# Optimization experiments

Hardware: AMD Instinct MI355X
Metric: run time of the kernel (lower is better)

The kernel has to match this reference:

```python
import jax, jax.numpy as jnp
import numpy as np
from itertools import permutations

N_NODES, B, C, H, W = 3, 4, 256, 40, 40
NO_PASS = 2


def _conv3x3(x, w, b):
    # x: [NB, Cin, H, W], w: [Cout, Cin, 3, 3]
    y = jax.lax.conv_general_dilated(
        x, w, window_strides=(1, 1), padding='SAME',
        dimension_numbers=('NCHW', 'OIHW', 'NCHW'))
    return y + b[None, :, None, None]


def setup_inputs() -> dict:
    key = jax.random.key(0)
    ks = jax.random.split(key, 7)
    s = 0.02
    return {
        'nodes': jax.random.normal(ks[0], (N_NODES, B, C, H, W), jnp.float32),
        'theta_w': jax.random.normal(ks[1], (C, C), jnp.float32) * s,
        'theta_b': jax.random.normal(ks[2], (C,), jnp.float32) * s,
        'gru_gates_w': jax.random.normal(ks[3], (2 * C, 2 * C, 3, 3), jnp.float32) * s,
        'gru_gates_b': jax.random.normal(ks[4], (2 * C,), jnp.float32) * s,
        'gru_can_w': jax.random.normal(ks[5], (C, 2 * C, 3, 3), jnp.float32) * s,
        'gru_can_b': jax.random.normal(ks[6], (C,), jnp.float32) * s,
    }


def reference(nodes, theta_w, theta_b, gru_gates_w, gru_gates_b, gru_can_w, gru_can_b):
    N, Bn, Cn, Hn, Wn = nodes.shape
    P = Hn * Wn
    edges = np.array(list(permutations(range(N), 2)))  # [E, 2]
    recv = jnp.asarray(edges[:, 0])  # edge[0] receives message
    send = jnp.asarray(edges[:, 1])  # edge[1] sends

    for _ in range(NO_PASS):
        nf = nodes.reshape(N, Bn, Cn, P)
        # theta is a 1x1 conv == channel matmul
        th = jnp.einsum('oc,nbcp->nbop', theta_w, nf) + theta_b[None, None, :, None]
        thi = th[recv]          # [E, B, C, P]
        ei = nf[recv]           # [E, B, C, P]
        ej = nf[send]           # [E, B, C, P]
        # scores[e,b,p,q] = theta(e1)[:,p] . e2[:,q]
        scores = jnp.einsum('ebcp,ebcq->ebpq', thi, ej)
        atn = jax.nn.softmax(scores, axis=-1)
        # message = atn @ (e2 + e1)^T, back to channel-first
        msg = jnp.einsum('ebpq,ebcq->ebcp', atn, ej + ei)  # [E, B, C, P]
        agg = jax.ops.segment_sum(msg, recv, num_segments=N)  # sum of incoming msgs

        # ConvGRU update, nodes folded into batch dim
        x = agg.reshape(N * Bn, Cn, Hn, Wn)
        h = nodes.reshape(N * Bn, Cn, Hn, Wn)
        gates = _conv3x3(jnp.concatenate([x, h], axis=1), gru_gates_w, gru_gates_b)
        r, z = jnp.split(jax.nn.sigmoid(gates), 2, axis=1)
        cand = jnp.tanh(_conv3x3(jnp.concatenate([x, r * h], axis=1), gru_can_w, gru_can_b))
        h_new = (1.0 - z) * h + z * cand
        nodes = h_new.reshape(N, Bn, Cn, Hn, Wn)
    return nodes
```

## Files before the change

kernel.cpp:

```cpp
#include <hip/hip_runtime.h>
#include <hip/hip_bf16.h>
#include <math.h>

#define NN 3
#define BB 4
#define CC 256
#define C2 512
#define HH 40
#define WW 40
#define PP 1600
#define NBB 12
#define NODESZ (NBB*CC*PP)
#define TO 16
#define PAD 1764

typedef short short8 __attribute__((ext_vector_type(8)));
typedef float f32x4 __attribute__((ext_vector_type(4)));
typedef unsigned short ushort_t;
typedef unsigned int uint_t;

__device__ __forceinline__ ushort_t f2bf(float x) {
  union { float f; uint_t u; } v; v.f = x;
  uint_t r = v.u + 0x7fff + ((v.u >> 16) & 1);
  return (ushort_t)(r >> 16);
}

__device__ __forceinline__ void async_ld16(const ushort_t* g, ushort_t* l) {
  __builtin_amdgcn_global_load_lds(
      (const __attribute__((address_space(1))) uint_t*)g,
      (__attribute__((address_space(3))) uint_t*)l, 16, 0, 0);
}

__global__ void k_copy(const float* __restrict__ in, float* __restrict__ out) {
  int i = blockIdx.x * 256 + threadIdx.x;
  out[i] = in[i];
}

__global__ void k_theta(const float* __restrict__ nodes, const float* __restrict__ tw,
                        const float* __restrict__ tb, ushort_t* __restrict__ th_t) {
  __shared__ float w[TO * CC];
  int t = threadIdx.x;
  int nb = blockIdx.y / (CC / TO);
  int o0 = (blockIdx.y % (CC / TO)) * TO;
  for (int i = t; i < TO * CC; i += 320) w[i] = tw[(o0 + (i >> 8)) * CC + (i & 255)];
  __syncthreads();
  int p = blockIdx.x * 320 + t;
  const float* src = nodes + nb * CC * PP + p;
  float acc[TO];
#pragma unroll
  for (int o = 0; o < TO; ++o) acc[o] = tb[o0 + o];
  for (int c = 0; c < CC; c += 4) {
    float v0 = src[c * PP], v1 = src[(c + 1) * PP], v2 = src[(c + 2) * PP], v3 = src[(c + 3) * PP];
#pragma unroll
    for (int o = 0; o < TO; ++o) {
      const float4 ww = *(const float4*)(w + o * CC + c);
      acc[o] += ww.x * v0 + ww.y * v1 + ww.z * v2 + ww.w * v3;
    }
  }
  size_t base = ((size_t)nb * PP + p) * CC + o0;
#pragma unroll
  for (int o = 0; o < TO; o += 2) {
    uint_t lo = f2bf(acc[o]), hi = f2bf(acc[o + 1]);
    *(uint_t*)&th_t[base + o] = lo | (hi << 16);
  }
}

__global__ void k_to_bf_t(const float* __restrict__ src, ushort_t* __restrict__ dst) {
  __shared__ float tile[32][33];
  int nb = blockIdx.z;
  int c0 = blockIdx.y * 32;
  int pp0 = blockIdx.x * 32;
  int tx = threadIdx.x & 31, ty = threadIdx.x >> 5;
#pragma unroll
  for (int i = 0; i < 4; ++i)
    tile[ty + 8 * i][tx] = src[((size_t)nb * CC + c0 + ty + 8 * i) * PP + pp0 + tx];
  __syncthreads();
#pragma unroll
  for (int i = 0; i < 4; ++i) {
    int q = pp0 + ty + 8 * i;
    int c = c0 + tx;
    int cs = c ^ ((q & 7) << 3);
    dst[((size_t)nb * PP + q) * CC + cs] = f2bf(tile[tx][ty + 8 * i]);
  }
}

__global__ void k_prep_vf(const float* __restrict__ nodes, ushort_t* __restrict__ vf) {
  int T = blockIdx.x;
  int eb = blockIdx.y;
  int e = eb >> 2, b = eb & 3;
  int n = e >> 1, jidx = e & 1;
  int js = jidx + (jidx >= n ? 1 : 0);
  const float* s0 = nodes + (size_t)(n * BB + b) * CC * PP;
  const float* s1 = nodes + (size_t)(js * BB + b) * CC * PP;
  ushort_t* dst = vf + ((size_t)eb * 50 + T) * 8192;
  int t = threadIdx.x;
#pragma unroll
  for (int k = 0; k < 4; ++k) {
    int cid = t + 256 * k;
    int nt = cid >> 6, l = cid & 63;
    int quad = l >> 4, l16 = l & 15;
    int c = 16 * nt + l16;
    int p = 32 * T + quad * 8;
    const float4* a0 = (const float4*)(s0 + (size_t)c * PP + p);
    const float4* a1 = (const float4*)(s1 + (size_t)c * PP + p);
    float4 x0 = a0[0], x1 = a0[1];
    float4 y0 = a1[0], y1 = a1[1];
    short8 o;
    o[0] = (short)f2bf(x0.x + y0.x); o[1] = (short)f2bf(x0.y + y0.y);
    o[2] = (short)f2bf(x0.z + y0.z); o[3] = (short)f2bf(x0.w + y0.w);
    o[4] = (short)f2bf(x1.x + y1.x); o[5] = (short)f2bf(x1.y + y1.y);
    o[6] = (short)f2bf(x1.z + y1.z); o[7] = (short)f2bf(x1.w + y1.w);
    *(short8*)(dst + (size_t)cid * 8) = o;
  }
}

__global__ __launch_bounds__(256, 2) void k_attn_mfma(
    const ushort_t* __restrict__ nodes_bf_t,
    const ushort_t* __restrict__ th_t,
    const ushort_t* __restrict__ vf,
    float* __restrict__ agg_t)
{
  __shared__ ushort_t Ej[32 * 256];
  __shared__ ushort_t Sp[64 * 40];
  __shared__ float Al[64];
  __shared__ float Linv[64];

  const int t = threadIdx.x;
  const int w = t >> 6;
  const int l = t & 63;
  const int quad = l >> 4;
  const int l16 = l & 15;
  const int p0 = blockIdx.x * 64;
  const int nb = blockIdx.y;
  const int jidx = blockIdx.z;
  const int n = nb >> 2, b = nb & 3;
  const int e = n * 2 + jidx;
  const int js = jidx + (jidx >= n ? 1 : 0);
  const int eb = e * BB + b;

  const ushort_t* ejb = nodes_bf_t + ((size_t)(js * BB + b) * PP) * CC;
  const ushort_t* vbase = vf + (size_t)eb * 50 * 8192;

  short8 Ath[8];
  {
    const ushort_t* arow = th_t + ((size_t)nb * PP + p0 + 16 * w + l16) * CC + quad * 8;
#pragma unroll
    for (int ks = 0; ks < 8; ++ks) Ath[ks] = *(const short8*)(arow + ks * 32);
  }

  float M = -3.0e38f, Lr = 0.f;
  f32x4 O[4][4];
#pragma unroll
  for (int mt = 0; mt < 4; ++mt)
#pragma unroll
    for (int nt = 0; nt < 4; ++nt)
#pragma unroll
      for (int r = 0; r < 4; ++r) O[mt][nt][r] = 0.f;

#pragma unroll
  for (int i = 0; i < 4; ++i)
    async_ld16(ejb + (4 * w + i) * 512 + l * 8, &Ej[(4 * w + i) * 512]);

  for (int T = 0; T < 50; ++T) {
    __syncthreads();
    short8 Bv[4];
    {
      const ushort_t* vt = vbase + (size_t)T * 8192;
#pragma unroll
      for (int nt = 0; nt < 4; ++nt)
        Bv[nt] = *(const short8*)(vt + (4 * w + nt) * 512 + l * 8);
    }
    f32x4 S0, S1;
#pragma unroll
    for (int r = 0; r < 4; ++r) { S0[r] = 0.f; S1[r] = 0.f; }
#pragma unroll
    for (int ks = 0; ks < 8; ++ks) {
      int ch0 = (((ks * 4 + quad) ^ (l16 & 7)) << 3);
      short8 A0 = *(const short8*)(Ej + l16 * CC + ch0);
      short8 A1 = *(const short8*)(Ej + (16 + l16) * CC + ch0);
      S0 = __builtin_amdgcn_mfma_f32_16x16x32_bf16(A0, Ath[ks], S0, 0, 0, 0);
      S1 = __builtin_amdgcn_mfma_f32_16x16x32_bf16(A1, Ath[ks], S1, 0, 0, 0);
    }
    float m = fmaxf(fmaxf(fmaxf(S0[0], S0[1]), fmaxf(S0[2], S0[3])),
                    fmaxf(fmaxf(S1[0], S1[1]), fmaxf(S1[2], S1[3])));
    m = fmaxf(m, __shfl_xor(m, 16));
    m = fmaxf(m, __shfl_xor(m, 32));
    float Mn = fmaxf(M, m);
    float al = __expf(M - Mn);
    float e0 = __expf(S0[0] - Mn), e1 = __expf(S0[1] - Mn);
    float e2 = __expf(S0[2] - Mn), e3 = __expf(S0[3] - Mn);
    float e4 = __expf(S1[0] - Mn), e5 = __expf(S1[1] - Mn);
    float e6 = __expf(S1[2] - Mn), e7 = __expf(S1[3] - Mn);
    float s = ((e0 + e1) + (e2 + e3)) + ((e4 + e5) + (e6 + e7));
    s += __shfl_xor(s, 16);
    s += __shfl_xor(s, 32);
    Lr = Lr * al + s;
    M = Mn;
    {
      uint2 u;
      u.x = (uint_t)f2bf(e0) | ((uint_t)f2bf(e1) << 16);
      u.y = (uint_t)f2bf(e2) | ((uint_t)f2bf(e3) << 16);
      *(uint2*)&Sp[(16 * w + l16) * 40 + quad * 4] = u;
      uint2 v;
      v.x = (uint_t)f2bf(e4) | ((uint_t)f2bf(e5) << 16);
      v.y = (uint_t)f2bf(e6) | ((uint_t)f2bf(e7) << 16);
      *(uint2*)&Sp[(16 * w + l16) * 40 + 16 + quad * 4] = v;
      if (quad == 0) Al[16 * w + l16] = al;
    }
    __syncthreads();
    if (T < 49) {
#pragma unroll
      for (int i = 0; i < 4; ++i)
        async_ld16(ejb + (size_t)(T + 1) * 8192 + (4 * w + i) * 512 + l * 8,
                   &Ej[(4 * w + i) * 512]);
    }
#pragma unroll
    for (int mt = 0; mt < 4; ++mt) {
      f32x4 a4 = *(const f32x4*)&Al[16 * mt + quad * 4];
#pragma unroll
      for (int nt = 0; nt < 4; ++nt)
#pragma unroll
        for (int r = 0; r < 4; ++r) O[mt][nt][r] *= a4[r];
    }
#pragma unroll
    for (int mt = 0; mt < 4; ++mt) {
      short8 Ap = *(const short8*)&Sp[(16 * mt + l16) * 40 + quad * 8];
#pragma unroll
      for (int nt = 0; nt < 4; ++nt)
        O[mt][nt] = __builtin_amdgcn_mfma_f32_16x16x32_bf16(Ap, Bv[nt], O[mt][nt], 0, 0, 0);
    }
  }
  __syncthreads();
  if (quad == 0) Linv[16 * w + l16] = 1.f / Lr;
  __syncthreads();
  float* ao = agg_t + (((size_t)jidx * NBB + nb) * PP + p0) * CC;
#pragma unroll
  for (int mt = 0; mt < 4; ++mt) {
    f32x4 li = *(const f32x4*)&Linv[16 * mt + quad * 4];
#pragma unroll
    for (int r = 0; r < 4; ++r) {
      float* dst = ao + (size_t)(16 * mt + quad * 4 + r) * CC + 64 * w + l16;
#pragma unroll
      for (int nt = 0; nt < 4; ++nt) dst[16 * nt] = O[mt][nt][r] * li[r];
    }
  }
}


__global__ void k_wrep(const float* __restrict__ w, ushort_t* __restrict__ wr) {
  int i = blockIdx.x * 256 + threadIdx.x;
  int ci = i & 511;
  int rest = i >> 9;
  int tp = rest % 9, co = rest / 9;
  wr[i] = f2bf(w[((size_t)co * 512 + ci) * 9 + tp]);
}

__global__ void k_pad_zero(ushort_t* __restrict__ xpad) {
  int i = blockIdx.x * 256 + threadIdx.x;
  xpad[i] = 0;
}

__global__ void k_pad_agg(const float* __restrict__ agg_t, ushort_t* __restrict__ xpad) {
  int i = blockIdx.x * 256 + threadIdx.x;
  int c = i & 255;
  int rest = i >> 8;
  int px = rest % PP, nb = rest / PP;
  int y = px / 40, x = px - y * 40;
  size_t src = ((size_t)nb * PP + px) * CC + c;
  float v = agg_t[src] + agg_t[(size_t)NBB * PP * CC + src];
  xpad[((size_t)nb * PAD + (y + 1) * 42 + (x + 1)) * C2 + c] = f2bf(v);
}

template <int MODE>
__global__ void k_pad_tr(const float* __restrict__ srcA, const float* __restrict__ srcB,
                         ushort_t* __restrict__ xpad) {
  __shared__ float tile[32][33];
  int nb = blockIdx.z;
  int c0 = blockIdx.y * 32;
  int pp0 = blockIdx.x * 32;
  int tx = threadIdx.x & 31, ty = threadIdx.x >> 5;
#pragma unroll
  for (int i = 0; i < 4; ++i) {
    int c = c0 + ty + 8 * i;
    float v = srcA[((size_t)nb * CC + c) * PP + pp0 + tx];
    if (MODE == 1) v *= srcB[((size_t)nb * C2 + c) * PP + pp0 + tx];
    tile[ty + 8 * i][tx] = v;
  }
  __syncthreads();
#pragma unroll
  for (int i = 0; i < 4; ++i) {
    int px = pp0 + ty + 8 * i;
    int y = px / 40, x = px - y * 40;
    xpad[((size_t)nb * PAD + (y + 1) * 42 + (x + 1)) * C2 + CC + c0 + tx] =
        f2bf(tile[tx][ty + 8 * i]);
  }
}

template <int ACT>
__global__ __launch_bounds__(256) void k_conv_mfma(
    const ushort_t* __restrict__ xpad,
    const ushort_t* __restrict__ wr,
    const float* __restrict__ bias,
    const float* __restrict__ zsrc,
    float* __restrict__ out)
{
  __shared__ ushort_t Asm[128 * 32];
  __shared__ ushort_t Bsm[128 * 32];
  const int t = threadIdx.x;
  const int w = t >> 6, l = t & 63, quad = l >> 4, l16 = l & 15;
  const int nb = blockIdx.z;
  const int m0 = blockIdx.y * 128;
  const int px0 = blockIdx.x * 128;
  const int wm = (w >> 1) * 64, wn = (w & 1) * 64;

  const int lr = l >> 2;
  const int swf = (lr ^ (lr >> 2)) & 3;
  const int lk = ((l & 3) ^ swf) * 8;
  const ushort_t* wsrc = wr + (size_t)(m0 + 32 * w + lr) * 4608 + lk;
  int pxa = px0 + 32 * w + lr;      if (pxa > 1599) pxa = 1599;
  int pxb = pxa + 16;               if (pxb > 1599) pxb = 1599;
  {
    int d = px0 + 32 * w + 16 + lr; if (d <= 1599) pxb = d;
  }
  const int ya = pxa / 40, xa = pxa - ya * 40;
  const int yb = pxb / 40, xb = pxb - yb * 40;
  const ushort_t* bsrc_a = xpad + ((size_t)nb * PAD + ya * 42 + xa) * C2 + lk;
  const ushort_t* bsrc_b = xpad + ((size_t)nb * PAD + yb * 42 + xb) * C2 + lk;
  ushort_t* Ad0 = Asm + w * 1024;
  ushort_t* Ad1 = Asm + w * 1024 + 512;
  ushort_t* Bd0 = Bsm + w * 1024;
  ushort_t* Bd1 = Bsm + w * 1024 + 512;

  const int swr = (l16 ^ (l16 >> 2)) & 3;
  const int fk = ((quad ^ swr) * 8);

  f32x4 acc[4][4];
#pragma unroll
  for (int mt = 0; mt < 4; ++mt)
#pragma unroll
    for (int nt = 0; nt < 4; ++nt)
#pragma unroll
      for (int r = 0; r < 4; ++r) acc[mt][nt][r] = 0.f;

  for (int tap = 0; tap < 9; ++tap) {
    const int ky = tap / 3, kx = tap - ky * 3;
    const int boff = (ky * 42 + kx) * C2;
    const ushort_t* wtap = wsrc + tap * 512;
#pragma unroll 1
    for (int c0 = 0; c0 < 512; c0 += 32) {
      __syncthreads();
      async_ld16(wtap + c0, Ad0);
      async_ld16(wtap + 16 * 4608 + c0, Ad1);
      async_ld16(bsrc_a + boff + c0, Bd0);
      async_ld16(bsrc_b + boff + c0, Bd1);
      __syncthreads();
      short8 Af[4], Bf[4];
#pragma unroll
      for (int mt = 0; mt < 4; ++mt)
        Af[mt] = *(const short8*)(Asm + (wm + mt * 16 + l16) * 32 + fk);
#pragma unroll
      for (int nt = 0; nt < 4; ++nt)
        Bf[nt] = *(const short8*)(Bsm + (wn + nt * 16 + l16) * 32 + fk);
#pragma unroll
      for (int mt = 0; mt < 4; ++mt)
#pragma unroll
        for (int nt = 0; nt < 4; ++nt)
          acc[mt][nt] = __builtin_amdgcn_mfma_f32_16x16x32_bf16(Af[mt], Bf[nt], acc[mt][nt], 0, 0, 0);
    }
  }

#pragma unroll
  for (int mt = 0; mt < 4; ++mt) {
#pragma unroll
    for (int r = 0; r < 4; ++r) {
      int co = m0 + wm + mt * 16 + quad * 4 + r;
      float bv = bias[co];
#pragma unroll
      for (int nt = 0; nt < 4; ++nt) {
        int px = px0 + wn + nt * 16 + l16;
        if (px >= PP) continue;
        float v = acc[mt][nt][r] + bv;
        if (ACT == 0) {
          out[((size_t)nb * C2 + co) * PP + px] = 1.f / (1.f + __expf(-v));
        } else {
          v = tanhf(v);
          float z = zsrc[((size_t)nb * C2 + CC + co) * PP + px];
          float* hp = out + ((size_t)nb * CC + co) * PP + px;
          float h = *hp;
          *hp = (1.f - z) * h + z * v;
        }
      }
    }
  }
}

extern "C" void kernel_launch(void* const* d_in, const int* in_sizes, int n_in,
                              void* d_out, int out_size, void* d_ws, size_t ws_size,
                              hipStream_t stream) {
  const float* nodes_in = (const float*)d_in[0];
  const float* tw = (const float*)d_in[1];
  const float* tb = (const float*)d_in[2];
  const float* gw = (const float*)d_in[3];
  const float* gb = (const float*)d_in[4];
  const float* cw = (const float*)d_in[5];
  const float* cb = (const float*)d_in[6];

  float* nodes = (float*)d_out;
  char* ws = (char*)d_ws;
  ushort_t* nodes_bf_t = (ushort_t*)ws;
  ushort_t* th_t  = (ushort_t*)(ws + 9830400);
  ushort_t* vf    = (ushort_t*)(ws + 19660800);
  float*    agg_t = (float*)(ws + 39321600);
  ushort_t* xh_pad = (ushort_t*)(ws + 9830400);
  float*    gates = (float*)(ws + 39321600);
  ushort_t* w_g_r = (ushort_t*)(ws + 78643200);
  ushort_t* w_c_r = (ushort_t*)(ws + 83361792);

  k_copy<<<NODESZ / 256, 256, 0, stream>>>(nodes_in, nodes);
  k_wrep<<<(C2 * 9 * C2) / 256, 256, 0, stream>>>(gw, w_g_r);
  k_wrep<<<(CC * 9 * C2) / 256, 256, 0, stream>>>(cw, w_c_r);
  for (int pass = 0; pass < 2; ++pass) {
    k_theta<<<dim3(5, NBB * (CC / TO)), 320, 0, stream>>>(nodes, tw, tb, th_t);
    k_to_bf_t<<<dim3(50, 8, NBB), 256, 0, stream>>>(nodes, nodes_bf_t);
    k_prep_vf<<<dim3(50, 24), 256, 0, stream>>>(nodes, vf);
    k_attn_mfma<<<dim3(25, NBB, 2), 256, 0, stream>>>(nodes_bf_t, th_t, vf, agg_t);
    k_pad_zero<<<(NBB * PAD * C2) / 256, 256, 0, stream>>>(xh_pad);
    k_pad_agg<<<(NBB * PP * CC) / 256, 256, 0, stream>>>(agg_t, xh_pad);
    k_pad_tr<0><<<dim3(50, 8, NBB), 256, 0, stream>>>(nodes, nullptr, xh_pad);
    k_conv_mfma<0><<<dim3(13, 4, NBB), 256, 0, stream>>>(xh_pad, w_g_r, gb, nullptr, gates);
    k_pad_tr<1><<<dim3(50, 8, NBB), 256, 0, stream>>>(nodes, gates, xh_pad);
    k_conv_mfma<1><<<dim3(13, 2, NBB), 256, 0, stream>>>(xh_pad, w_c_r, cb, gates, nodes);
  }
}
```

Measured before the change: 1.107 ms.

## Double-buffer LDS tiles in MFMA conv to overlap loads with compute

Splits the A and B shared-memory tiles into two buffers and flattens the tap and channel loops into a single 144-step loop. Each step issues the async global-to-LDS loads for the next K-slice while the MFMAs run on the current slice. This leaves one barrier per step instead of two and is meant to hide global load latency. The cost is twice the LDS footprint, which may lower occupancy, and correctness relies on the barrier also waiting for the outstanding async loads.

Result: no change. 1.111 ms (+0.4%).

```diff
diff --git a/kernel.cpp b/kernel.cpp
--- a/kernel.cpp
+++ b/kernel.cpp
@@ -304,8 +304,8 @@
     const float* __restrict__ zsrc,
     float* __restrict__ out)
 {
-  __shared__ ushort_t Asm[128 * 32];
-  __shared__ ushort_t Bsm[128 * 32];
+  __shared__ ushort_t Asm[2][128 * 32];
+  __shared__ ushort_t Bsm[2][128 * 32];
   const int t = threadIdx.x;
   const int w = t >> 6, l = t & 63, quad = l >> 4, l16 = l & 15;
   const int nb = blockIdx.z;
@@ -326,10 +326,6 @@
   const int yb = pxb / 40, xb = pxb - yb * 40;
   const ushort_t* bsrc_a = xpad + ((size_t)nb * PAD + ya * 42 + xa) * C2 + lk;
   const ushort_t* bsrc_b = xpad + ((size_t)nb * PAD + yb * 42 + xb) * C2 + lk;
-  ushort_t* Ad0 = Asm + w * 1024;
-  ushort_t* Ad1 = Asm + w * 1024 + 512;
-  ushort_t* Bd0 = Bsm + w * 1024;
-  ushort_t* Bd1 = Bsm + w * 1024 + 512;
 
   const int swr = (l16 ^ (l16 >> 2)) & 3;
   const int fk = ((quad ^ swr) * 8);
@@ -342,31 +338,37 @@
 #pragma unroll
       for (int r = 0; r < 4; ++r) acc[mt][nt][r] = 0.f;
 
-  for (int tap = 0; tap < 9; ++tap) {
-    const int ky = tap / 3, kx = tap - ky * 3;
-    const int boff = (ky * 42 + kx) * C2;
-    const ushort_t* wtap = wsrc + tap * 512;
+  auto stage = [&](int buf, int it) {
+    int tap = it >> 4;
+    int cc = (it & 15) << 5;
+    int ky = tap / 3, kx = tap - ky * 3;
+    int boff = (ky * 42 + kx) * C2 + cc;
+    const ushort_t* wtap = wsrc + tap * 512 + cc;
+    async_ld16(wtap, &Asm[buf][w * 1024]);
+    async_ld16(wtap + 16 * 4608, &Asm[buf][w * 1024 + 512]);
+    async_ld16(bsrc_a + boff, &Bsm[buf][w * 1024]);
+    async_ld16(bsrc_b + boff, &Bsm[buf][w * 1024 + 512]);
+  };
+
+  stage(0, 0);
+  int cur = 0;
 #pragma unroll 1
-    for (int c0 = 0; c0 < 512; c0 += 32) {
-      __syncthreads();
-      async_ld16(wtap + c0, Ad0);
-      async_ld16(wtap + 16 * 4608 + c0, Ad1);
-      async_ld16(bsrc_a + boff + c0, Bd0);
-      async_ld16(bsrc_b + boff + c0, Bd1);
-      __syncthreads();
-      short8 Af[4], Bf[4];
-#pragma unroll
-      for (int mt = 0; mt < 4; ++mt)
-        Af[mt] = *(const short8*)(Asm + (wm + mt * 16 + l16) * 32 + fk);
+  for (int it = 0; it < 144; ++it) {
+    __syncthreads();
+    if (it + 1 < 144) stage(cur ^ 1, it + 1);
+    short8 Af[4], Bf[4];
+#pragma unroll
+    for (int mt = 0; mt < 4; ++mt)
+      Af[mt] = *(const short8*)(&Asm[cur][0] + (wm + mt * 16 + l16) * 32 + fk);
+#pragma unroll
+    for (int nt = 0; nt < 4; ++nt)
+      Bf[nt] = *(const short8*)(&Bsm[cur][0] + (wn + nt * 16 + l16) * 32 + fk);
+#pragma unroll
+    for (int mt = 0; mt < 4; ++mt)
 #pragma unroll
       for (int nt = 0; nt < 4; ++nt)
-        Bf[nt] = *(const short8*)(Bsm + (wn + nt * 16 + l16) * 32 + fk);
-#pragma unroll
-      for (int mt = 0; mt < 4; ++mt)
-#pragma unroll
-        for (int nt = 0; nt < 4; ++nt)
-          acc[mt][nt] = __builtin_amdgcn_mfma_f32_16x16x32_bf16(Af[mt], Bf[nt], acc[mt][nt], 0, 0, 0);
-    }
+        acc[mt][nt] = __builtin_amdgcn_mfma_f32_16x16x32_bf16(Af[mt], Bf[nt], acc[mt][nt], 0, 0, 0);
+    cur ^= 1;
   }
 
 #pragma unroll
```
